# Performance work log

Measured on AMD Instinct MI355X. Metric: run time of the kernel, lower is better.

## Reference

```python
import jax, jax.numpy as jnp
import numpy as np

D_MODEL = 1024
NHEAD = 16
HEAD_DIM = D_MODEL // NHEAD
D_FF = 4096
EPS = 1e-5


def _layer_norm(x, gamma, beta):
    mu = jnp.mean(x, axis=-1, keepdims=True)
    var = jnp.mean((x - mu) ** 2, axis=-1, keepdims=True)
    return (x - mu) * jax.lax.rsqrt(var + EPS) * gamma + beta


def setup_inputs() -> dict:
    key = jax.random.key(0)
    ks = jax.random.split(key, 12)
    B, S = 2, 2048
    s = lambda fan_in: 1.0 / np.sqrt(fan_in)
    return {
        "src": jax.random.normal(ks[0], (B, S, D_MODEL), dtype=jnp.float32),
        "attn_bias": jax.random.normal(ks[1], (NHEAD, S, S), dtype=jnp.float32) * 0.02,
        "qkv_w": jax.random.uniform(ks[2], (3 * D_MODEL, D_MODEL), minval=-s(D_MODEL), maxval=s(D_MODEL)),
        "qkv_b": jax.random.uniform(ks[3], (3 * D_MODEL,), minval=-s(D_MODEL), maxval=s(D_MODEL)),
        "out_w": jax.random.uniform(ks[4], (D_MODEL, D_MODEL), minval=-s(D_MODEL), maxval=s(D_MODEL)),
        "out_b": jax.random.uniform(ks[5], (D_MODEL,), minval=-s(D_MODEL), maxval=s(D_MODEL)),
        "lin1_w": jax.random.uniform(ks[6], (D_FF, D_MODEL), minval=-s(D_MODEL), maxval=s(D_MODEL)),
        "lin1_b": jax.random.uniform(ks[7], (D_FF,), minval=-s(D_MODEL), maxval=s(D_MODEL)),
        "lin2_w": jax.random.uniform(ks[8], (D_MODEL, D_FF), minval=-s(D_FF), maxval=s(D_FF)),
        "lin2_b": jax.random.uniform(ks[9], (D_MODEL,), minval=-s(D_FF), maxval=s(D_FF)),
        "ln1_g": jnp.ones((D_MODEL,)), "ln1_b": jnp.zeros((D_MODEL,)),
        "ln2_g": jnp.ones((D_MODEL,)), "ln2_b": jnp.zeros((D_MODEL,)),
    }


def reference(src, attn_bias, qkv_w, qkv_b, out_w, out_b, lin1_w, lin1_b,
              lin2_w, lin2_b, ln1_g, ln1_b, ln2_g, ln2_b):
    B, S, _ = src.shape
    qkv = src @ qkv_w.T + qkv_b                      # [B,S,3D]
    q, k, v = jnp.split(qkv, 3, axis=-1)
    q = q.reshape(B, S, NHEAD, HEAD_DIM)
    k = k.reshape(B, S, NHEAD, HEAD_DIM)
    v = v.reshape(B, S, NHEAD, HEAD_DIM)
    scores = jnp.einsum('bthd,bshd->bhts', q, k) / np.sqrt(HEAD_DIM)
    scores = scores + attn_bias[None]                # 3D bias -> broadcast over batch
    weights = jax.nn.softmax(scores, axis=-1)
    ctx = jnp.einsum('bhts,bshd->bthd', weights, v).reshape(B, S, D_MODEL)
    attn_out = ctx @ out_w.T + out_b
    x = _layer_norm(src + attn_out, ln1_g, ln1_b)
    ff = jax.nn.gelu(x @ lin1_w.T + lin1_b, approximate=False) @ lin2_w.T + lin2_b
    return _layer_norm(x + ff, ln2_g, ln2_b)
```

## Files before the change

### kernel.cpp

```cpp
#include <hip/hip_runtime.h>
#include <hip/hip_bf16.h>


#define DMODEL 1024
#define NHEAD  16
#define HD     64
#define DFF    4096
#define SEQ    2048
#define BATCH  2
#define TOKD   ((size_t)4096 * 1024)

using short8 = __attribute__((ext_vector_type(8))) short;
using f32x4  = __attribute__((ext_vector_type(4))) float;
typedef unsigned short bfu;

__device__ __forceinline__ bfu f2bf(float f) {
    unsigned int u = __float_as_uint(f);
    unsigned int r = (u + 0x7fffu + ((u >> 16) & 1u)) >> 16;
    return (bfu)r;
}

__device__ __forceinline__ float gelu_exact(float x) {
    return 0.5f * x * (1.0f + erff(x * 0.70710678118654752f));
}

__device__ __forceinline__ void gload16(const void* g, void* l) {
    __builtin_amdgcn_global_load_lds(
        (const __attribute__((address_space(1))) void*)g,
        (__attribute__((address_space(3))) void*)l, 16, 0, 0);
}

__device__ __forceinline__ int swz(int row, int colbyte) {
    return (row * 128 + colbyte) ^ ((row & 7) << 4);
}

struct CvtPack {
    const float* in[5];
    bfu* out[5];
    unsigned start[6];
};

__global__ __launch_bounds__(256) void cvt_multi(CvtPack p) {
    unsigned gid = blockIdx.x * 256 + threadIdx.x;
    if (gid >= p.start[5]) return;
    int i = 0;
    #pragma unroll
    for (int k = 1; k < 5; ++k) i += (gid >= p.start[k]);
    unsigned local = gid - p.start[i];
    float4 v = *(const float4*)(p.in[i] + (size_t)local * 4);
    uint2 o;
    o.x = (unsigned)f2bf(v.x) | ((unsigned)f2bf(v.y) << 16);
    o.y = (unsigned)f2bf(v.z) | ((unsigned)f2bf(v.w) << 16);
    *(uint2*)(p.out[i] + (size_t)local * 4) = o;
}

template <int MODE, int BM, int SPLITK>
__global__ __launch_bounds__(256) void gemm_bt(const bfu* __restrict__ A,
                                               const bfu* __restrict__ W,
                                               const float* __restrict__ bias,
                                               void* __restrict__ Cout,
                                               int M, int N, int K) {
    constexpr int MR = BM / 32;
    __shared__ __align__(16) bfu As[2][BM * 32];
    __shared__ __align__(16) bfu Bs[2][128 * 32];
    const int tid = threadIdx.x;
    const int wid = tid >> 6, lane = tid & 63;
    const int lg = lane >> 4, li = lane & 15;

    const int nx = gridDim.x;
    int wg = blockIdx.x + nx * blockIdx.y;
    const int nwg = nx * gridDim.y;
    {
        const int qq = nwg >> 3, rr = nwg & 7;
        const int xcd = wg & 7, idx = wg >> 3;
        wg = (xcd < rr ? xcd * (qq + 1) : rr * (qq + 1) + (xcd - rr) * qq) + idx;
    }
    const int row0 = (wg % nx) * BM, col0 = (wg / nx) * 128;
    const int wr = (wid >> 1) * (BM / 2), wc = (wid & 1) * 64;
    f32x4 acc[MR][4] = {};

    const int kchunk = K / SPLITK;
    const int kbeg = blockIdx.z * kchunk;

    const int ch_row = tid >> 2;
    const int ch_col = (tid & 3) * 8;
    const bfu* Ag0 = A + (size_t)(row0 + ch_row) * K + kbeg + ch_col;
    const bfu* Ag1 = A + (size_t)(row0 + 64 + ch_row) * K + kbeg + ch_col;
    const bfu* Wg0 = W + (size_t)(col0 + ch_row) * K + kbeg + ch_col;
    const bfu* Wg1 = W + (size_t)(col0 + 64 + ch_row) * K + kbeg + ch_col;

    auto stage = [&](int buf, int k0) {
        gload16(Ag0 + k0, (char*)As[buf] + wid * 1024);
        if constexpr (BM == 128) gload16(Ag1 + k0, (char*)As[buf] + 4096 + wid * 1024);
        gload16(Wg0 + k0, (char*)Bs[buf] + wid * 1024);
        gload16(Wg1 + k0, (char*)Bs[buf] + 4096 + wid * 1024);
    };

    stage(0, 0);
    __syncthreads();
    int cur = 0;
    for (int k0 = 0; k0 < kchunk; k0 += 32) {
        if (k0 + 32 < kchunk) stage(cur ^ 1, k0 + 32);
        short8 af[MR], bf_[4];
        #pragma unroll
        for (int m = 0; m < MR; ++m)
            af[m] = *(const short8*)(As[cur] + (wr + m * 16 + li) * 32 + lg * 8);
        #pragma unroll
        for (int n = 0; n < 4; ++n)
            bf_[n] = *(const short8*)(Bs[cur] + (wc + n * 16 + li) * 32 + lg * 8);
        #pragma unroll
        for (int m = 0; m < MR; ++m)
            #pragma unroll
            for (int n = 0; n < 4; ++n)
                acc[m][n] = __builtin_amdgcn_mfma_f32_16x16x32_bf16(af[m], bf_[n], acc[m][n], 0, 0, 0);
        __syncthreads();
        cur ^= 1;
    }

    float* Cp3 = (float*)Cout + (size_t)blockIdx.z * M * N;
    #pragma unroll
    for (int m = 0; m < MR; ++m) {
        #pragma unroll
        for (int n = 0; n < 4; ++n) {
            #pragma unroll
            for (int r = 0; r < 4; ++r) {
                int row = row0 + wr + m * 16 + lg * 4 + r;
                int col = col0 + wc + n * 16 + li;
                if (MODE == 3) {
                    Cp3[(size_t)row * N + col] = acc[m][n][r];
                } else {
                    float v = acc[m][n][r] + bias[col];
                    if (MODE == 2) v = gelu_exact(v);
                    ((bfu*)Cout)[(size_t)row * N + col] = f2bf(v);
                }
            }
        }
    }
}

__global__ __launch_bounds__(256) void attn_kernel(const bfu* __restrict__ qkv,
                                                   const float* __restrict__ bias,
                                                   bfu* __restrict__ ctx) {
    __shared__ __align__(16) bfu Ks[128 * 64];
    __shared__ __align__(16) bfu Vt[2][64 * 64];
    __shared__ __align__(16) bfu Ps[4][16 * 64];
    const int tid = threadIdx.x;
    const int wid = tid >> 6, lane = tid & 63;
    const int lg = lane >> 4, li = lane & 15;
    const int q0 = blockIdx.x * 64;
    const int bh = blockIdx.y;
    const int h = bh >> 1, b = bh & 1;
    const size_t tokbase = (size_t)b * SEQ;

    short8 qa[2];
    {
        const bfu* qp = qkv + (tokbase + q0 + wid * 16 + li) * 3072 + h * 64;
        qa[0] = *(const short8*)(qp + lg * 8);
        qa[1] = *(const short8*)(qp + 32 + lg * 8);
    }

    f32x4 o[4] = {};
    float mrow[4], lrow[4];
    #pragma unroll
    for (int r = 0; r < 4; ++r) { mrow[r] = -1e30f; lrow[r] = 0.f; }

    char* pb = (char*)Ps[wid];
    const float* brow = bias + (size_t)h * SEQ * SEQ;
    const int qrbase = q0 + wid * 16 + lg * 4;

    const int krow  = tid >> 3;
    const int kcolb = (tid & 7) * 16;

    for (int kt = 0; kt < SEQ; kt += 128) {
        #pragma unroll
        for (int p = 0; p < 4; ++p) {
            int r_ = p * 32 + krow;
            uint4 v = *(const uint4*)(qkv + (tokbase + kt + r_) * 3072 + 1024 + h * 64 + (kcolb >> 1));
            *(uint4*)((char*)Ks + swz(r_, kcolb)) = v;
        }
        #pragma unroll
        for (int jh = 0; jh < 2; ++jh) {
            #pragma unroll
            for (int i = 0; i < 2; ++i) {
                int jb = i * 4 + wid;
                bfu tmp[8];
                #pragma unroll
                for (int u = 0; u < 8; ++u)
                    tmp[u] = qkv[(tokbase + kt + jh * 64 + jb * 8 + u) * 3072 + 2048 + h * 64 + lane];
                uint4 pv;
                pv.x = (unsigned)tmp[0] | ((unsigned)tmp[1] << 16);
                pv.y = (unsigned)tmp[2] | ((unsigned)tmp[3] << 16);
                pv.z = (unsigned)tmp[4] | ((unsigned)tmp[5] << 16);
                pv.w = (unsigned)tmp[6] | ((unsigned)tmp[7] << 16);
                *(uint4*)((char*)Vt[jh] + swz(lane, jb * 16)) = pv;
            }
        }
        __syncthreads();

        float breg[4][8];
        #pragma unroll
        for (int r = 0; r < 4; ++r) {
            const float* bq = brow + (size_t)(qrbase + r) * SEQ + kt;
            #pragma unroll
            for (int nb = 0; nb < 8; ++nb)
                breg[r][nb] = bq[nb * 16 + li];
        }

        f32x4 s[8] = {};
        __builtin_amdgcn_s_setprio(1);
        #pragma unroll
        for (int cb = 0; cb < 2; ++cb) {
            #pragma unroll
            for (int nb = 0; nb < 8; ++nb) {
                short8 kf = *(const short8*)((char*)Ks + swz(nb * 16 + li, cb * 64 + lg * 16));
                s[nb] = __builtin_amdgcn_mfma_f32_16x16x32_bf16(qa[cb], kf, s[nb], 0, 0, 0);
            }
        }
        __builtin_amdgcn_s_setprio(0);

        #pragma unroll
        for (int r = 0; r < 4; ++r) {
            float sv[8];
            float mx = -1e30f;
            #pragma unroll
            for (int nb = 0; nb < 8; ++nb) {
                float v = s[nb][r] * 0.125f + breg[r][nb];
                sv[nb] = v;
                mx = fmaxf(mx, v);
            }
            #pragma unroll
            for (int off = 8; off; off >>= 1) mx = fmaxf(mx, __shfl_xor(mx, off));
            float mnew = fmaxf(mrow[r], mx);
            float sf = __expf(mrow[r] - mnew);
            mrow[r] = mnew;
            float rs = 0.f;
            #pragma unroll
            for (int nb = 0; nb < 8; ++nb) {
                float p = __expf(sv[nb] - mnew);
                rs += p;
                s[nb][r] = p;
            }
            #pragma unroll
            for (int off = 8; off; off >>= 1) rs += __shfl_xor(rs, off);
            lrow[r] = lrow[r] * sf + rs;
            #pragma unroll
            for (int dc = 0; dc < 4; ++dc) o[dc][r] *= sf;
        }

        #pragma unroll
        for (int jh = 0; jh < 2; ++jh) {
            #pragma unroll
            for (int nb = 0; nb < 4; ++nb)
                #pragma unroll
                for (int r = 0; r < 4; ++r)
                    *(bfu*)(pb + swz(lg * 4 + r, (nb * 16 + li) * 2)) = f2bf(s[jh * 4 + nb][r]);
            __builtin_amdgcn_s_setprio(1);
            #pragma unroll
            for (int jb = 0; jb < 2; ++jb) {
                short8 pa = *(const short8*)(pb + swz(li, jb * 64 + lg * 16));
                short8 vb[4];
                #pragma unroll
                for (int dc = 0; dc < 4; ++dc)
                    vb[dc] = *(const short8*)((char*)Vt[jh] + swz(dc * 16 + li, jb * 64 + lg * 16));
                #pragma unroll
                for (int dc = 0; dc < 4; ++dc)
                    o[dc] = __builtin_amdgcn_mfma_f32_16x16x32_bf16(pa, vb[dc], o[dc], 0, 0, 0);
            }
            __builtin_amdgcn_s_setprio(0);
        }
        __syncthreads();
    }

    #pragma unroll
    for (int dc = 0; dc < 4; ++dc)
        #pragma unroll
        for (int r = 0; r < 4; ++r) {
            int qr = qrbase + r;
            int d = dc * 16 + li;
            float v = o[dc][r] / lrow[r];
            ctx[(tokbase + qr) * 1024 + h * 64 + d] = f2bf(v);
        }
}

template <int P>
__global__ __launch_bounds__(256) void residual_lnP(const float* __restrict__ a,
                                                    const float* __restrict__ parts,
                                                    const float* __restrict__ pbias,
                                                    const float* __restrict__ g,
                                                    const float* __restrict__ be,
                                                    float* __restrict__ xf,
                                                    bfu* __restrict__ xb) {
    const int row = blockIdx.x, t = threadIdx.x;
    const size_t off = (size_t)row * DMODEL + t * 4;
    float4 v = *(const float4*)(a + off);
    #pragma unroll
    for (int i = 0; i < P; ++i) {
        float4 p = *(const float4*)(parts + i * TOKD + off);
        v.x += p.x; v.y += p.y; v.z += p.z; v.w += p.w;
    }
    float4 pb = *(const float4*)(pbias + t * 4);
    v.x += pb.x; v.y += pb.y; v.z += pb.z; v.w += pb.w;

    float s  = v.x + v.y + v.z + v.w;
    float sq = v.x * v.x + v.y * v.y + v.z * v.z + v.w * v.w;
    #pragma unroll
    for (int o2 = 32; o2; o2 >>= 1) { s += __shfl_xor(s, o2); sq += __shfl_xor(sq, o2); }
    __shared__ float red[8];
    const int wid = t >> 6, lane = t & 63;
    if (lane == 0) { red[wid] = s; red[4 + wid] = sq; }
    __syncthreads();
    s  = red[0] + red[1] + red[2] + red[3];
    sq = red[4] + red[5] + red[6] + red[7];
    float mu  = s * (1.0f / DMODEL);
    float var = sq * (1.0f / DMODEL) - mu * mu;
    float rstd = rsqrtf(var + 1e-5f);
    float4 gv  = *(const float4*)(g + t * 4);
    float4 bev = *(const float4*)(be + t * 4);
    float4 ov;
    ov.x = (v.x - mu) * rstd * gv.x + bev.x;
    ov.y = (v.y - mu) * rstd * gv.y + bev.y;
    ov.z = (v.z - mu) * rstd * gv.z + bev.z;
    ov.w = (v.w - mu) * rstd * gv.w + bev.w;
    *(float4*)(xf + off) = ov;
    if (xb) {
        uint2 o;
        o.x = (unsigned)f2bf(ov.x) | ((unsigned)f2bf(ov.y) << 16);
        o.y = (unsigned)f2bf(ov.z) | ((unsigned)f2bf(ov.w) << 16);
        *(uint2*)(xb + off) = o;
    }
}

extern "C" void kernel_launch(void* const* d_in, const int* in_sizes, int n_in,
                              void* d_out, int out_size, void* d_ws, size_t ws_size,
                              hipStream_t stream) {
    const float* src    = (const float*)d_in[0];
    const float* abias  = (const float*)d_in[1];
    const float* qkv_w  = (const float*)d_in[2];
    const float* qkv_b  = (const float*)d_in[3];
    const float* out_w  = (const float*)d_in[4];
    const float* out_b  = (const float*)d_in[5];
    const float* lin1_w = (const float*)d_in[6];
    const float* lin1_b = (const float*)d_in[7];
    const float* lin2_w = (const float*)d_in[8];
    const float* lin2_b = (const float*)d_in[9];
    const float* ln1_g  = (const float*)d_in[10];
    const float* ln1_b  = (const float*)d_in[11];
    const float* ln2_g  = (const float*)d_in[12];
    const float* ln2_b  = (const float*)d_in[13];
    float* out = (float*)d_out;

    const int T = BATCH * SEQ;
    char* w = (char*)d_ws;
    auto take = [&](size_t bytes) { char* p = w; w += (bytes + 255) & ~(size_t)255; return p; };
    bfu*   src_bf  = (bfu*)take((size_t)T * DMODEL * 2);
    bfu*   qkvw_bf = (bfu*)take((size_t)3 * DMODEL * DMODEL * 2);
    bfu*   outw_bf = (bfu*)take((size_t)DMODEL * DMODEL * 2);
    bfu*   l1w_bf  = (bfu*)take((size_t)DFF * DMODEL * 2);
    bfu*   l2w_bf  = (bfu*)take((size_t)DMODEL * DFF * 2);
    bfu*   qkv_bf  = (bfu*)take((size_t)T * 3 * DMODEL * 2);
    bfu*   ctx_bf  = (bfu*)take((size_t)T * DMODEL * 2);
    float* outp_p  = (float*)take((size_t)2 * T * DMODEL * 4);
    float* x_f     = (float*)take((size_t)T * DMODEL * 4);
    bfu*   x_bf    = (bfu*)take((size_t)T * DMODEL * 2);
    bfu*   h1_bf   = (bfu*)take((size_t)T * DFF * 2);
    float* l2_p    = (float*)take((size_t)2 * T * DMODEL * 4);

    {
        CvtPack p;
        p.in[0] = src;    p.out[0] = src_bf;
        p.in[1] = qkv_w;  p.out[1] = qkvw_bf;
        p.in[2] = out_w;  p.out[2] = outw_bf;
        p.in[3] = lin1_w; p.out[3] = l1w_bf;
        p.in[4] = lin2_w; p.out[4] = l2w_bf;
        unsigned n4[5] = {
            (unsigned)((size_t)T * DMODEL / 4),
            (unsigned)((size_t)3 * DMODEL * DMODEL / 4),
            (unsigned)((size_t)DMODEL * DMODEL / 4),
            (unsigned)((size_t)DFF * DMODEL / 4),
            (unsigned)((size_t)DMODEL * DFF / 4)};
        p.start[0] = 0;
        for (int i = 0; i < 5; ++i) p.start[i + 1] = p.start[i] + n4[i];
        cvt_multi<<<(p.start[5] + 255) / 256, 256, 0, stream>>>(p);
    }

    gemm_bt<0, 128, 1><<<dim3(T / 128, (3 * DMODEL) / 128, 1), 256, 0, stream>>>(
        src_bf, qkvw_bf, qkv_b, qkv_bf, T, 3 * DMODEL, DMODEL);
    attn_kernel<<<dim3(SEQ / 64, BATCH * NHEAD), 256, 0, stream>>>(qkv_bf, abias, ctx_bf);
    gemm_bt<3, 64, 2><<<dim3(T / 64, DMODEL / 128, 2), 256, 0, stream>>>(
        ctx_bf, outw_bf, nullptr, outp_p, T, DMODEL, DMODEL);
    residual_lnP<2><<<T, 256, 0, stream>>>(src, outp_p, out_b, ln1_g, ln1_b, x_f, x_bf);
    gemm_bt<2, 128, 1><<<dim3(T / 128, DFF / 128, 1), 256, 0, stream>>>(
        x_bf, l1w_bf, lin1_b, h1_bf, T, DFF, DMODEL);
    gemm_bt<3, 64, 2><<<dim3(T / 64, DMODEL / 128, 2), 256, 0, stream>>>(
        h1_bf, l2w_bf, nullptr, l2_p, T, DMODEL, DFF);
    residual_lnP<2><<<T, 256, 0, stream>>>(x_f, l2_p, lin2_b, ln2_g, ln2_b, out, nullptr);
}
```

Before: 364.5 us.

## Drop fp32 residual buffer, truncate P to bf16, split attention barrier

The first LayerNorm no longer writes an fp32 copy of x. The second residual LayerNorm reads the bf16 x instead, cutting global traffic by about 24 MB. In the attention kernel, the full __syncthreads becomes an LDS-only wait plus barrier placed after the bias loads, so those global loads can overlap the barrier. P is converted to bf16 by truncation rather than rounding, and the final normalisation uses a reciprocal. Using bf16 for the residual input and truncating P both lower precision.

```diff
diff --git a/kernel.cpp b/kernel.cpp
--- a/kernel.cpp
+++ b/kernel.cpp
@@ -195,7 +195,6 @@
                 *(uint4*)((char*)Vt[jh] + swz(lane, jb * 16)) = pv;
             }
         }
-        __syncthreads();
 
         float breg[4][8];
         #pragma unroll
@@ -205,6 +204,9 @@
             for (int nb = 0; nb < 8; ++nb)
                 breg[r][nb] = bq[nb * 16 + li];
         }
+
+        asm volatile("s_waitcnt lgkmcnt(0)" ::: "memory");
+        __builtin_amdgcn_s_barrier();
 
         f32x4 s[8] = {};
         __builtin_amdgcn_s_setprio(1);
@@ -253,7 +255,8 @@
             for (int nb = 0; nb < 4; ++nb)
                 #pragma unroll
                 for (int r = 0; r < 4; ++r)
-                    *(bfu*)(pb + swz(lg * 4 + r, (nb * 16 + li) * 2)) = f2bf(s[jh * 4 + nb][r]);
+                    *(bfu*)(pb + swz(lg * 4 + r, (nb * 16 + li) * 2)) =
+                        (bfu)(__float_as_uint(s[jh * 4 + nb][r]) >> 16);
             __builtin_amdgcn_s_setprio(1);
             #pragma unroll
             for (int jb = 0; jb < 2; ++jb) {
@@ -271,19 +274,22 @@
         __syncthreads();
     }
 
+    float il[4];
+    #pragma unroll
+    for (int r = 0; r < 4; ++r) il[r] = __builtin_amdgcn_rcpf(lrow[r]);
     #pragma unroll
     for (int dc = 0; dc < 4; ++dc)
         #pragma unroll
         for (int r = 0; r < 4; ++r) {
             int qr = qrbase + r;
             int d = dc * 16 + li;
-            float v = o[dc][r] / lrow[r];
+            float v = o[dc][r] * il[r];
             ctx[(tokbase + qr) * 1024 + h * 64 + d] = f2bf(v);
         }
 }
 
-template <int P>
-__global__ __launch_bounds__(256) void residual_lnP(const float* __restrict__ a,
+template <int P, bool ABF>
+__global__ __launch_bounds__(256) void residual_lnP(const void* __restrict__ a,
                                                     const float* __restrict__ parts,
                                                     const float* __restrict__ pbias,
                                                     const float* __restrict__ g,
@@ -292,7 +298,16 @@
                                                     bfu* __restrict__ xb) {
     const int row = blockIdx.x, t = threadIdx.x;
     const size_t off = (size_t)row * DMODEL + t * 4;
-    float4 v = *(const float4*)(a + off);
+    float4 v;
+    if constexpr (ABF) {
+        uint2 u = *(const uint2*)((const bfu*)a + off);
+        v.x = __uint_as_float((u.x & 0xffffu) << 16);
+        v.y = __uint_as_float(u.x & 0xffff0000u);
+        v.z = __uint_as_float((u.y & 0xffffu) << 16);
+        v.w = __uint_as_float(u.y & 0xffff0000u);
+    } else {
+        v = *(const float4*)((const float*)a + off);
+    }
     #pragma unroll
     for (int i = 0; i < P; ++i) {
         float4 p = *(const float4*)(parts + i * TOKD + off);
@@ -321,7 +336,7 @@
     ov.y = (v.y - mu) * rstd * gv.y + bev.y;
     ov.z = (v.z - mu) * rstd * gv.z + bev.z;
     ov.w = (v.w - mu) * rstd * gv.w + bev.w;
-    *(float4*)(xf + off) = ov;
+    if (xf) *(float4*)(xf + off) = ov;
     if (xb) {
         uint2 o;
         o.x = (unsigned)f2bf(ov.x) | ((unsigned)f2bf(ov.y) << 16);
@@ -360,7 +375,6 @@
     bfu*   qkv_bf  = (bfu*)take((size_t)T * 3 * DMODEL * 2);
     bfu*   ctx_bf  = (bfu*)take((size_t)T * DMODEL * 2);
     float* outp_p  = (float*)take((size_t)2 * T * DMODEL * 4);
-    float* x_f     = (float*)take((size_t)T * DMODEL * 4);
     bfu*   x_bf    = (bfu*)take((size_t)T * DMODEL * 2);
     bfu*   h1_bf   = (bfu*)take((size_t)T * DFF * 2);
     float* l2_p    = (float*)take((size_t)2 * T * DMODEL * 4);
@@ -388,10 +402,12 @@
     attn_kernel<<<dim3(SEQ / 64, BATCH * NHEAD), 256, 0, stream>>>(qkv_bf, abias, ctx_bf);
     gemm_bt<3, 64, 2><<<dim3(T / 64, DMODEL / 128, 2), 256, 0, stream>>>(
         ctx_bf, outw_bf, nullptr, outp_p, T, DMODEL, DMODEL);
-    residual_lnP<2><<<T, 256, 0, stream>>>(src, outp_p, out_b, ln1_g, ln1_b, x_f, x_bf);
+    residual_lnP<2, false><<<T, 256, 0, stream>>>(src, outp_p, out_b, ln1_g, ln1_b,
+                                                  nullptr, x_bf);
     gemm_bt<2, 128, 1><<<dim3(T / 128, DFF / 128, 1), 256, 0, stream>>>(
         x_bf, l1w_bf, lin1_b, h1_bf, T, DFF, DMODEL);
     gemm_bt<3, 64, 2><<<dim3(T / 64, DMODEL / 128, 2), 256, 0, stream>>>(
         h1_bf, l2w_bf, nullptr, l2_p, T, DMODEL, DFF);
-    residual_lnP<2><<<T, 256, 0, stream>>>(x_f, l2_p, lin2_b, ln2_g, ln2_b, out, nullptr);
-}
+    residual_lnP<2, true><<<T, 256, 0, stream>>>(x_bf, l2_p, lin2_b, ln2_g, ln2_b,
+                                                 out, nullptr);
+}
```

After: 353.9 us. 2.9% less time.
